# Kernel optimization log

Hardware: AMD Instinct MI355X
Metric: run time of the kernel (lower is better)

The kernel has to match this reference:

```python
import jax, jax.numpy as jnp
import numpy as np

B, DIM, IN_DIM, H, W = 4, 256, 128, 128, 128
DD = IN_DIM // 2          # down_dim = 64
HEADS = 8
BN_EPS = 1e-5


def conv2d(x, w, b=None, pad=0, dil=1):
    y = jax.lax.conv_general_dilated(
        x, w, window_strides=(1, 1),
        padding=[(pad, pad), (pad, pad)],
        rhs_dilation=(dil, dil),
        dimension_numbers=('NCHW', 'OIHW', 'NCHW'))
    if b is not None:
        y = y + b[None, :, None, None]
    return y


def bn_relu(x, s, o):
    # eval-mode BatchNorm2d with running_mean=0, running_var=1
    return jax.nn.relu(x * (s / np.sqrt(1.0 + BN_EPS))[None, :, None, None] + o[None, :, None, None])


def setup_inputs() -> dict:
    ks = iter(jax.random.split(jax.random.key(0), 80))

    def w(shape, sc=0.05):
        return sc * jax.random.normal(next(ks), shape, jnp.float32)

    def s(c):
        return 1.0 + 0.1 * jax.random.normal(next(ks), (c,), jnp.float32)

    def o(c):
        return 0.02 * jax.random.normal(next(ks), (c,), jnp.float32)

    d = {}
    d['x'] = jax.random.normal(next(ks), (B, DIM, H, W), jnp.float32)
    d['w_dc'] = w((IN_DIM, DIM, 3, 3)); d['b_dc'] = w((IN_DIM,)); d['s_dc'] = s(IN_DIM); d['o_dc'] = o(IN_DIM)
    d['w1'] = w((DD, IN_DIM, 1, 1)); d['b1'] = w((DD,)); d['s1'] = s(DD); d['o1'] = o(DD)
    d['w2'] = w((DD, DD, 3, 3)); d['b2'] = w((DD,)); d['s2'] = s(DD); d['o2'] = o(DD)
    d['w3'] = w((DD, DD, 3, 3)); d['b3'] = w((DD,)); d['s3'] = s(DD); d['o3'] = o(DD)
    d['w4'] = w((DD, DD, 3, 3)); d['b4'] = w((DD,)); d['s4'] = s(DD); d['o4'] = o(DD)
    d['w5'] = w((DD, IN_DIM, 1, 1)); d['b5'] = w((DD,)); d['s5'] = s(DD); d['o5'] = o(DD)
    d['temperature'] = jnp.ones((HEADS, 1, 1), jnp.float32)
    d['w_po'] = w((DD, 2 * DD, 1, 1))  # project_out, bias=False
    d['w_wa'] = w((DD // 16, DD, 1, 1)); d['b_wa'] = w((DD // 16,)); d['s_wa'] = s(DD // 16); d['o_wa'] = o(DD // 16)
    d['w_wb'] = w((DD, DD // 16, 1, 1)); d['b_wb'] = w((DD,))
    d['w_f'] = w((DD, 5 * DD, 1, 1)); d['b_f'] = w((DD,)); d['s_f'] = s(DD); d['o_f'] = o(DD)
    d['w_oa'] = w((DD // 2, DD, 3, 3)); d['b_oa'] = w((DD // 2,)); d['s_oa'] = s(DD // 2); d['o_oa'] = o(DD // 2)
    d['w_ob'] = w((1, DD // 2, 1, 1)); d['b_ob'] = w((1,))
    return d


def reference(x, w_dc, b_dc, s_dc, o_dc, w1, b1, s1, o1, w2, b2, s2, o2,
              w3, b3, s3, o3, w4, b4, s4, o4, w5, b5, s5, o5,
              temperature, w_po, w_wa, b_wa, s_wa, o_wa, w_wb, b_wb,
              w_f, b_f, s_f, o_f, w_oa, b_oa, s_oa, o_oa, w_ob, b_ob):

    def branch(c):
        b, ch, h, wd = c.shape
        f = jnp.fft.fft2(c)                                   # [b,ch,h,w] complex64 (q=k=v=tepqkv)
        qkv = f.reshape(b, HEADS, ch // HEADS, h * wd)        # v (unnormalized)
        n = jnp.sqrt(jnp.sum(jnp.square(jnp.abs(qkv)), axis=-1, keepdims=True))
        qn = qkv / jnp.maximum(n, 1e-12)                      # F.normalize(dim=-1); q == k
        attn = jnp.einsum('bhcn,bhdn->bhcd', qn, qn) * temperature
        # custom complex normalization: separate real/imag softmax
        attn = jax.lax.complex(jax.nn.softmax(attn.real, axis=-1),
                               jax.nn.softmax(attn.imag, axis=-1))
        of = jnp.abs(jnp.fft.ifft2(jnp.einsum('bhcd,bhdn->bhcn', attn, qkv)))  # ifft2 over (c, hw)
        of = of.reshape(b, ch, h, wd)
        g = jax.nn.sigmoid(conv2d(bn_relu(conv2d(f.real, w_wa, b_wa), s_wa, o_wa), w_wb, b_wb))
        ol = jnp.abs(jnp.fft.ifft2(g * f))                    # ifft2 over (h, w)
        return conv2d(jnp.concatenate([of, ol], axis=1), w_po) + c

    xd = bn_relu(conv2d(x, w_dc, b_dc, pad=1), s_dc, o_dc)
    c1 = bn_relu(conv2d(xd, w1, b1), s1, o1)
    c2 = bn_relu(conv2d(c1, w2, b2, pad=3, dil=3), s2, o2)
    F2 = branch(c2)
    c3 = bn_relu(conv2d(c1 + F2, w3, b3, pad=5, dil=5), s3, o3)
    F3 = branch(c3)
    c4 = bn_relu(conv2d(c1 + F3, w4, b4, pad=7, dil=7), s4, o4)
    F4 = branch(c4)
    # conv5: global avg pool -> 1x1 conv -> bilinear upsample of a 1x1 map == broadcast
    c5 = bn_relu(conv2d(jnp.mean(xd, axis=(2, 3), keepdims=True), w5, b5), s5, o5)
    c5 = jnp.broadcast_to(c5, (c5.shape[0], c5.shape[1], xd.shape[2], xd.shape[3]))
    fused = bn_relu(conv2d(jnp.concatenate([c1, F2, F3, F4, c5], axis=1), w_f, b_f), s_f, o_f)
    return conv2d(bn_relu(conv2d(fused, w_oa, b_oa, pad=1), s_oa, o_oa), w_ob, b_ob)
```

## Files before the change

kernel.cpp:

```cpp
#include <hip/hip_runtime.h>

#define S 16384
#define PI_F 3.14159265358979f

struct Ptrs { const float* p[43]; };

enum : int {
  O_SBDC=0, O_SB1=256, O_SB2=512, O_SB3=768, O_SB4=1024, O_SB5=1280,
  O_SBWA=1536, O_SBF=1792, O_SBOA=2048,
  O_M=2304, O_C5=2816, O_NRM=3072, O_GRAM=3328, O_ATT2=7424, O_BEFF=11520,
  O_WB=16384,
  O_PART=147456,
  O_H=180224,
  O_WP=442368,
  O_A=524288,
  O_FIN=8912896,
  O_CC=25690112,
  O_DRE=29884416, O_DIMG=34078720,
  O_ERE=38273024, O_EIM=42467328,
  O_G=46661632
};

typedef short bfrag __attribute__((ext_vector_type(8)));
typedef float ffrag __attribute__((ext_vector_type(4)));

__device__ __forceinline__ float bf2f(unsigned short u){
  union { unsigned int i; float f; } v; v.i = ((unsigned int)u) << 16; return v.f;
}
__device__ __forceinline__ unsigned short f2bf(float f){
  unsigned int x = __float_as_uint(f);
  unsigned int r = x + 0x7fffu + ((x >> 16) & 1u);
  return (unsigned short)(r >> 16);
}

__global__ void prep_sb_kernel(Ptrs P, float* ws){
  const float r = rsqrtf(1.0f + 1e-5f);
  int bi=0, si=0, oi=0, C=0, dst=0;
  switch (blockIdx.x){
    case 0: bi=2; si=3; oi=4; C=128; dst=O_SBDC; break;
    case 1: bi=6; si=7; oi=8; C=64; dst=O_SB1; break;
    case 2: bi=10; si=11; oi=12; C=64; dst=O_SB2; break;
    case 3: bi=14; si=15; oi=16; C=64; dst=O_SB3; break;
    case 4: bi=18; si=19; oi=20; C=64; dst=O_SB4; break;
    case 5: bi=22; si=23; oi=24; C=64; dst=O_SB5; break;
    case 6: bi=28; si=29; oi=30; C=4;  dst=O_SBWA; break;
    case 7: bi=34; si=35; oi=36; C=64; dst=O_SBF; break;
    default: bi=38; si=39; oi=40; C=32; dst=O_SBOA; break;
  }
  for (int c = threadIdx.x; c < C; c += 256){
    float bb = P.p[bi][c], ss = P.p[si][c], oo = P.p[oi][c];
    float sc = ss * r;
    ws[dst + c] = sc;
    ws[dst + C + c] = bb * sc + oo;
  }
}

__global__ __launch_bounds__(256) void xpad_kernel(const float* __restrict__ x,
    unsigned short* __restrict__ XT){
  int yy = blockIdx.x, b = blockIdx.y;
  long obase = ((long)(b*130) + yy) * (130L*256);
  int tid = threadIdx.x;
  if (yy == 0 || yy == 129){
    uint4 z; z.x=0; z.y=0; z.z=0; z.w=0;
    for (int i = tid; i < 130*256/8; i += 256)
      *(uint4*)(XT + obase + (long)i*8) = z;
    return;
  }
  __shared__ float LT[64][129];
  int y = yy - 1;
  for (int c0 = 0; c0 < 256; c0 += 64){
    for (int idx = tid; idx < 64*128; idx += 256){
      int ci = idx >> 7, xx = idx & 127;
      LT[ci][xx] = x[((long)(b*256 + c0 + ci)*128 + y)*128 + xx];
    }
    __syncthreads();
    for (int idx = tid; idx < 128*16; idx += 256){
      int xp = idx >> 4, c4 = (idx & 15)*4;
      ushort4 v;
      v.x = f2bf(LT[c4][xp]);   v.y = f2bf(LT[c4+1][xp]);
      v.z = f2bf(LT[c4+2][xp]); v.w = f2bf(LT[c4+3][xp]);
      *(ushort4*)(XT + obase + (long)(xp+1)*256 + c0 + c4) = v;
    }
    __syncthreads();
  }
  if (tid < 64){
    ushort4 z; z.x=0; z.y=0; z.z=0; z.w=0;
    *(ushort4*)(XT + obase + tid*4) = z;
    *(ushort4*)(XT + obase + 129L*256 + tid*4) = z;
  }
}

__global__ void wt_kernel(const float* __restrict__ w, unsigned short* __restrict__ WH,
    unsigned short* __restrict__ WL){
  for (int e = blockIdx.x*256 + threadIdx.x; e < 294912; e += gridDim.x*256){
    int c32 = e & 31, co = (e >> 5) & 127, kc = (e >> 12) & 7, sh = e >> 15;
    int ky = sh / 3, kx = sh - ky*3;
    int ci = kc*32 + c32;
    float v = w[((long)(co*256 + ci)*3 + ky)*3 + kx];
    unsigned short h = f2bf(v);
    WH[e] = h;
    WL[e] = f2bf(v - bf2f(h));
  }
}

__global__ void wtg_kernel(Ptrs P, unsigned short* __restrict__ WB){
  const float* w; int cout; long off;
  switch (blockIdx.y){
    case 0: w = P.p[9];  cout = 64; off = 0;      break;
    case 1: w = P.p[13]; cout = 64; off = 73728;  break;
    case 2: w = P.p[17]; cout = 64; off = 147456; break;
    default: w = P.p[37]; cout = 32; off = 221184; break;
  }
  int total = 576*cout;
  unsigned short* WH = WB + off;
  unsigned short* WL = WH + total;
  for (int e = blockIdx.x*256 + threadIdx.x; e < total; e += gridDim.x*256){
    int c32 = e & 31;
    int co = (e >> 5) & (cout - 1);
    int kc = (e / (32*cout)) & 1;
    int sh = e / (64*cout);
    int ky = sh/3, kx = sh - ky*3;
    int ci = kc*32 + c32;
    float v = w[((long)(co*64 + ci)*3 + ky)*3 + kx];
    unsigned short h = f2bf(v);
    WH[e] = h;
    WL[e] = f2bf(v - bf2f(h));
  }
}

__global__ void wtp_kernel(Ptrs P, unsigned short* __restrict__ WP){
  const float* w; int KC, wstr; long off;
  switch (blockIdx.y){
    case 0: w = P.p[5];  KC = 4; wstr = 128; off = 0;     break;
    case 1: w = P.p[26]; KC = 4; wstr = 128; off = 16384; break;
    default: w = P.p[33]; KC = 8; wstr = 320; off = 32768; break;
  }
  int total = KC*64*32;
  unsigned short* WH = WP + off;
  unsigned short* WL = WH + total;
  for (int e = blockIdx.x*256 + threadIdx.x; e < total; e += gridDim.x*256){
    int c32 = e & 31, co = (e >> 5) & 63, kc = e >> 11;
    float v = w[(long)co*wstr + kc*32 + c32];
    unsigned short h = f2bf(v);
    WH[e] = h;
    WL[e] = f2bf(v - bf2f(h));
  }
}

template<int DIL>
__global__ __launch_bounds__(256) void xpad64_kernel(const float* __restrict__ in1,
    const float* __restrict__ in2, long in_bs, unsigned short* __restrict__ XP){
  constexpr int TW = 128 + 2*DIL;
  int yy = blockIdx.x, b = blockIdx.y;
  long obase = (long)(b*TW + yy) * TW * 64;
  int tid = threadIdx.x;
  if (yy < DIL || yy >= 128 + DIL){
    uint4 z; z.x=0; z.y=0; z.z=0; z.w=0;
    for (int i = tid; i < TW*8; i += 256)
      *(uint4*)(XP + obase + (long)i*8) = z;
    return;
  }
  __shared__ float LT[64][129];
  int y = yy - DIL;
  const float* p1 = in1 + (long)b*in_bs + (long)y*128;
  const float* p2 = in2 ? in2 + (long)b*in_bs + (long)y*128 : nullptr;
  for (int idx = tid; idx < 64*128; idx += 256){
    int ci = idx >> 7, xx = idx & 127;
    float v = p1[(long)ci*S + xx];
    if (p2) v += p2[(long)ci*S + xx];
    LT[ci][xx] = v;
  }
  __syncthreads();
  for (int i = tid; i < 2*DIL*16; i += 256){
    int side = i / (DIL*16);
    int r = i - side*(DIL*16);
    int xcol = side ? (128 + DIL + (r >> 4)) : (r >> 4);
    ushort4 z; z.x=0; z.y=0; z.z=0; z.w=0;
    *(ushort4*)(XP + obase + (long)xcol*64 + (r & 15)*4) = z;
  }
  for (int idx = tid; idx < 128*16; idx += 256){
    int xp = idx >> 4, c4 = (idx & 15)*4;
    ushort4 v;
    v.x = f2bf(LT[c4][xp]);   v.y = f2bf(LT[c4+1][xp]);
    v.z = f2bf(LT[c4+2][xp]); v.w = f2bf(LT[c4+3][xp]);
    *(ushort4*)(XP + obase + (long)(xp + DIL)*64 + c4) = v;
  }
}

template<int DIL, int KC, int NBLK>
__global__ __launch_bounds__(256) void conv3x3_mfma_kernel(
    const unsigned short* __restrict__ XP,
    const unsigned short* __restrict__ WH, const unsigned short* __restrict__ WL,
    const float* __restrict__ scbi, float* __restrict__ out){
  constexpr int CIN = KC*32;
  constexpr int TW = 128 + 2*DIL;
  constexpr int NJ = NBLK/32;
  constexpr int LDA = 36;
  __shared__ unsigned short As[TW*LDA];
  int bid = blockIdx.x;
  int y = (bid & 7)*16 + ((bid >> 3) & 15);
  int b = (bid >> 7) & 3;
  int n2 = bid >> 9;
  int nb = gridDim.x >> 9; if (nb == 0) nb = 1;
  int coutTotal = nb * NBLK;
  int tid = threadIdx.x, wv = tid >> 6, lane = tid & 63;
  int mhalf = wv & 1, nhalf = wv >> 1;
  int px0 = mhalf*64;
  ffrag acc[4][NJ];
  #pragma unroll
  for (int i = 0; i < 4; i++)
    #pragma unroll
    for (int j = 0; j < NJ; j++)
      #pragma unroll
      for (int r = 0; r < 4; r++) acc[i][j][r] = 0.f;

  int kq = (lane >> 4)*8, rown = lane & 15;
  int sx = tid >> 2, sq = tid & 3;
  int cobase = n2*NBLK + nhalf*(NBLK/2);

  for (int ky = 0; ky < 3; ky++){
    long rowbase = ((long)(b*TW + y + ky*DIL))*TW*CIN;
    for (int kc = 0; kc < KC; kc++){
      __syncthreads();
      for (int x = sx; x < TW; x += 64){
        uint4 v = *(const uint4*)(XP + rowbase + (long)x*CIN + kc*32 + sq*8);
        *(uint4*)&As[x*LDA + sq*8] = v;
      }
      __syncthreads();
      #pragma unroll
      for (int kx = 0; kx < 3; kx++){
        int step = (ky*3 + kx)*KC + kc;
        bfrag bhf[NJ], blf[NJ];
        #pragma unroll
        for (int j = 0; j < NJ; j++){
          long wb = ((long)step*coutTotal + cobase + j*16 + rown)*32 + kq;
          bhf[j] = *(const bfrag*)(WH + wb);
          blf[j] = *(const bfrag*)(WL + wb);
        }
        bfrag af[4];
        #pragma unroll
        for (int i = 0; i < 4; i++){
          int x = px0 + i*16 + rown + kx*DIL;
          af[i] = *(const bfrag*)&As[x*LDA + kq];
        }
        #pragma unroll
        for (int i = 0; i < 4; i++)
          #pragma unroll
          for (int j = 0; j < NJ; j++){
            acc[i][j] = __builtin_amdgcn_mfma_f32_16x16x32_bf16(af[i], blf[j], acc[i][j], 0, 0, 0);
            acc[i][j] = __builtin_amdgcn_mfma_f32_16x16x32_bf16(af[i], bhf[j], acc[i][j], 0, 0, 0);
          }
      }
    }
  }
  #pragma unroll
  for (int i = 0; i < 4; i++){
    int pixel = px0 + i*16 + (lane >> 4)*4;
    #pragma unroll
    for (int j = 0; j < NJ; j++){
      int co = cobase + j*16 + (lane & 15);
      float sc = scbi[co], bb = scbi[coutTotal + co];
      float* op = out + ((long)(b*coutTotal + co))*S + y*128 + pixel;
      #pragma unroll
      for (int r = 0; r < 4; r++)
        op[r] = fmaxf(acc[i][j][r]*sc + bb, 0.f);
    }
  }
}

template<int MODE, int KC, int BF16IN>
__global__ __launch_bounds__(256) void conv1x1_mfma_kernel(
    const void* __restrict__ inv, long in_bs,
    const unsigned short* __restrict__ WH, const unsigned short* __restrict__ WL,
    const float* __restrict__ scbi, const float* __restrict__ beff,
    const float* __restrict__ res, long res_bs,
    float* __restrict__ out, long out_bs){
  constexpr int LDA = 36;
  __shared__ unsigned short Als[128*LDA];
  __shared__ unsigned short BHs[64*LDA];
  __shared__ unsigned short BLs[64*LDA];
  int bid = blockIdx.x;
  int y = (bid & 7)*16 + ((bid >> 3) & 15);
  int b = bid >> 7;
  int tid = threadIdx.x, wv = tid >> 6, lane = tid & 63;
  int mt0 = (wv & 1)*4, nt0 = (wv >> 1)*2;
  ffrag acc[4][2];
  #pragma unroll
  for (int i = 0; i < 4; i++)
    #pragma unroll
    for (int j = 0; j < 2; j++)
      #pragma unroll
      for (int r = 0; r < 4; r++) acc[i][j][r] = 0.f;
  int pq = tid & 31, cg = tid >> 5;
  int kq = (lane >> 4)*8, rown = lane & 15;
  int wrB = (tid >> 2)*LDA + (tid & 3)*8;
  const float* ibf = (const float*)inv + (long)b*in_bs + y*128;
  const unsigned short* ibs = (const unsigned short*)inv + (long)b*in_bs + y*128;
  unsigned short a[16];
  uint4 BHr, BLr;
  #pragma unroll
  for (int cc = 0; cc < 4; cc++)
    #pragma unroll
    for (int i = 0; i < 4; i++){
      if (BF16IN) a[cc*4 + i] = ibs[(long)(cg*4 + cc)*S + pq + 32*i];
      else        a[cc*4 + i] = f2bf(ibf[(long)(cg*4 + cc)*S + pq + 32*i]);
    }
  BHr = *(const uint4*)(WH + tid*8);
  BLr = *(const uint4*)(WL + tid*8);
  for (int kc = 0; kc < KC; kc++){
    __syncthreads();
    #pragma unroll
    for (int i = 0; i < 4; i++){
      ushort4 v;
      v.x = a[0 + i];  v.y = a[4 + i];
      v.z = a[8 + i];  v.w = a[12 + i];
      *(ushort4*)&Als[(pq + 32*i)*LDA + cg*4] = v;
    }
    *(uint4*)&BHs[wrB] = BHr;
    *(uint4*)&BLs[wrB] = BLr;
    __syncthreads();
    if (kc + 1 < KC){
      #pragma unroll
      for (int cc = 0; cc < 4; cc++)
        #pragma unroll
        for (int i = 0; i < 4; i++){
          long off = (long)((kc + 1)*32 + cg*4 + cc)*S + pq + 32*i;
          if (BF16IN) a[cc*4 + i] = ibs[off];
          else        a[cc*4 + i] = f2bf(ibf[off]);
        }
      long gw = (long)(kc + 1)*2048;
      BHr = *(const uint4*)(WH + gw + tid*8);
      BLr = *(const uint4*)(WL + gw + tid*8);
    }
    bfrag af[4], bhf[2], blf[2];
    #pragma unroll
    for (int i = 0; i < 4; i++)
      af[i] = *(const bfrag*)&Als[((mt0 + i)*16 + rown)*LDA + kq];
    #pragma unroll
    for (int j = 0; j < 2; j++){
      bhf[j] = *(const bfrag*)&BHs[((nt0 + j)*16 + rown)*LDA + kq];
      blf[j] = *(const bfrag*)&BLs[((nt0 + j)*16 + rown)*LDA + kq];
    }
    #pragma unroll
    for (int i = 0; i < 4; i++)
      #pragma unroll
      for (int j = 0; j < 2; j++){
        acc[i][j] = __builtin_amdgcn_mfma_f32_16x16x32_bf16(af[i], blf[j], acc[i][j], 0, 0, 0);
        acc[i][j] = __builtin_amdgcn_mfma_f32_16x16x32_bf16(af[i], bhf[j], acc[i][j], 0, 0, 0);
      }
  }
  #pragma unroll
  for (int i = 0; i < 4; i++){
    int pixel = (mt0 + i)*16 + (lane >> 4)*4;
    #pragma unroll
    for (int j = 0; j < 2; j++){
      int co = (nt0 + j)*16 + (lane & 15);
      float* op = out + (long)b*out_bs + (long)co*S + y*128 + pixel;
      #pragma unroll
      for (int r = 0; r < 4; r++){
        float v = acc[i][j][r];
        if (MODE == 0){
          v = fmaxf(v*scbi[co] + scbi[64 + co], 0.f);
        } else if (MODE == 1){
          v += res[(long)b*res_bs + (long)co*S + y*128 + pixel + r];
        } else {
          v = fmaxf(v*scbi[co] + beff[b*64 + co], 0.f);
        }
        op[r] = v;
      }
    }
  }
}

__device__ __forceinline__ void fft128_mk_tw(float (&tws)[8], float (&twc)[8],
                                             float sign, int lane){
  float a0 = sign * (2.0f*PI_F/128.0f) * (float)lane;
  __sincosf(a0, &tws[0], &twc[0]);
  int i = 1;
  #pragma unroll
  for (int h = 32; h >= 1; h >>= 1, i++){
    int j = lane & (h - 1);
    float a = sign * (2.0f*PI_F/128.0f) * (float)(j * (64/h));
    __sincosf(a, &tws[i], &twc[i]);
  }
}

__device__ __forceinline__ void fft128(float& z0r, float& z0i, float& z1r, float& z1i,
    const float (&tws)[8], const float (&twc)[8], int lane){
  {
    float ar = z0r, ai = z0i, br = z1r, bi = z1i;
    z0r = ar + br; z0i = ai + bi;
    float dr = ar - br, di = ai - bi;
    float s = tws[0], c = twc[0];
    z1r = dr*c - di*s; z1i = dr*s + di*c;
  }
  int idx = 1;
  #pragma unroll
  for (int h = 32; h >= 1; h >>= 1, idx++){
    float s = tws[idx], c = twc[idx];
    bool up = (lane & h) != 0;
    float pr, pi, nr, ni;
    pr = __shfl_xor(z0r, h, 64); pi = __shfl_xor(z0i, h, 64);
    if (!up){ nr = z0r + pr; ni = z0i + pi; }
    else { float dr = pr - z0r, di = pi - z0i; nr = dr*c - di*s; ni = dr*s + di*c; }
    z0r = nr; z0i = ni;
    pr = __shfl_xor(z1r, h, 64); pi = __shfl_xor(z1i, h, 64);
    if (!up){ nr = z1r + pr; ni = z1i + pi; }
    else { float dr = pr - z1r, di = pi - z1i; nr = dr*c - di*s; ni = dr*s + di*c; }
    z1r = nr; z1i = ni;
  }
}


__global__ __launch_bounds__(1024) void fft2_fwd_kernel(const float* __restrict__ in,
    unsigned short* __restrict__ outRe, unsigned short* __restrict__ outIm){
  __shared__ float lre[128][129];
  __shared__ float lim[128][129];
  int plane = blockIdx.x;
  int tid = threadIdx.x, wv = tid >> 6, lane = tid & 63;
  long pbase = (long)plane * S;
  for (int i = tid; i < S/4; i += 1024){
    int px = i*4; int r = px >> 7, c = px & 127;
    float4 v = *(const float4*)(in + pbase + px);
    lre[r][c] = v.x; lre[r][c+1] = v.y; lre[r][c+2] = v.z; lre[r][c+3] = v.w;
  }
  float tws[8], twc[8];
  fft128_mk_tw(tws, twc, -1.0f, lane);
  __syncthreads();
  #pragma unroll
  for (int rr = 0; rr < 8; rr++){
    int r = wv*8 + rr;
    float z0r = lre[r][lane], z0i = 0.f;
    float z1r = lre[r][lane + 64], z1i = 0.f;
    fft128(z0r, z0i, z1r, z1i, tws, twc, lane);
    int k = __brev(lane) >> 25;
    lre[r][k] = z0r;     lim[r][k] = z0i;
    lre[r][k+1] = z1r;   lim[r][k+1] = z1i;
  }
  __syncthreads();
  #pragma unroll
  for (int cc = 0; cc < 8; cc++){
    int c = wv*8 + cc;
    float z0r = lre[lane][c], z0i = lim[lane][c];
    float z1r = lre[lane + 64][c], z1i = lim[lane + 64][c];
    fft128(z0r, z0i, z1r, z1i, tws, twc, lane);
    int k = __brev(lane) >> 25;
    lre[k][c] = z0r;     lim[k][c] = z0i;
    lre[k+1][c] = z1r;   lim[k+1][c] = z1i;
  }
  __syncthreads();
  for (int i = tid; i < S/2; i += 1024){
    int px = i*2; int r = px >> 7, c = px & 127;
    ushort2 vr, vi;
    vr.x = f2bf(lre[r][c]); vr.y = f2bf(lre[r][c+1]);
    vi.x = f2bf(lim[r][c]); vi.y = f2bf(lim[r][c+1]);
    *(ushort2*)(outRe + pbase + px) = vr;
    *(ushort2*)(outIm + pbase + px) = vi;
  }
}

__global__ __launch_bounds__(1024) void ifft2_gate_abs_ol_kernel(
    const unsigned short* __restrict__ Dre, const unsigned short* __restrict__ Dim,
    const float* __restrict__ H, const float* __restrict__ wb, const float* __restrict__ bwb,
    unsigned short* __restrict__ AB){
  __shared__ float lre[128][129];
  __shared__ float lim[128][129];
  int plane = blockIdx.x;
  int b = plane >> 6, ch = plane & 63;
  int tid = threadIdx.x, wv = tid >> 6, lane = tid & 63;
  long pbase = (long)plane * S;
  float w0 = wb[ch*4], w1 = wb[ch*4+1], w2 = wb[ch*4+2], w3 = wb[ch*4+3];
  float bw = bwb[ch];
  const float* Hb = H + (long)b*4*S;
  for (int i = tid; i < S; i += 1024){
    int r = i >> 7, c = i & 127;
    float hv = bw + w0*Hb[i] + w1*Hb[S + i] + w2*Hb[2*S + i] + w3*Hb[3*S + i];
    float g = 1.0f / (1.0f + __expf(-hv));
    lre[r][c] = bf2f(Dre[pbase + i]) * g;
    lim[r][c] = bf2f(Dim[pbase + i]) * g;
  }
  float tws[8], twc[8];
  fft128_mk_tw(tws, twc, 1.0f, lane);
  __syncthreads();
  #pragma unroll
  for (int cc = 0; cc < 8; cc++){
    int c = wv*8 + cc;
    float z0r = lre[lane][c], z0i = lim[lane][c];
    float z1r = lre[lane + 64][c], z1i = lim[lane + 64][c];
    fft128(z0r, z0i, z1r, z1i, tws, twc, lane);
    int k = __brev(lane) >> 25;
    lre[k][c] = z0r;     lim[k][c] = z0i;
    lre[k+1][c] = z1r;   lim[k+1][c] = z1i;
  }
  __syncthreads();
  unsigned short* out = AB + ((long)(b*128 + 64 + ch)) * S;
  #pragma unroll
  for (int rr = 0; rr < 8; rr++){
    int r = wv*8 + rr;
    float z0r = lre[r][lane], z0i = lim[r][lane];
    float z1r = lre[r][lane + 64], z1i = lim[r][lane + 64];
    fft128(z0r, z0i, z1r, z1i, tws, twc, lane);
    int k = __brev(lane) >> 25;
    ushort2 v;
    v.x = f2bf(sqrtf(z0r*z0r + z0i*z0i) * (1.0f/16384.0f));
    v.y = f2bf(sqrtf(z1r*z1r + z1i*z1i) * (1.0f/16384.0f));
    *(ushort2*)(out + (long)r*128 + k) = v;
  }
}

__global__ __launch_bounds__(1024) void ifft2_attn_abs_ofT_kernel(
    const unsigned short* __restrict__ Dre, const unsigned short* __restrict__ Dim,
    const float* __restrict__ ATT2, unsigned short* __restrict__ AB){
  __shared__ float lre[128][129];
  __shared__ float lim[128][129];
  int plane = blockIdx.x;
  int b = plane >> 6, ch = plane & 63;
  int bh = plane >> 3;
  int cp = plane & 7;
  int tid = threadIdx.x, wv = tid >> 6, lane = tid & 63;
  long hbase = (long)bh * 8 * S;
  float wr[8], wi[8];
  #pragma unroll
  for (int d = 0; d < 8; d++){
    wr[d] = ATT2[bh*128 + (cp*8 + d)*2];
    wi[d] = ATT2[bh*128 + (cp*8 + d)*2 + 1];
  }
  for (int i = tid; i < S/2; i += 1024){
    int px = i*2;
    float sr0=0.f, si0=0.f, sr1=0.f, si1=0.f;
    #pragma unroll
    for (int d = 0; d < 8; d++){
      ushort2 ur = *(const ushort2*)(Dre + hbase + (long)d*S + px);
      ushort2 ui = *(const ushort2*)(Dim + hbase + (long)d*S + px);
      float xr0 = bf2f(ur.x), xi0 = bf2f(ui.x);
      float xr1 = bf2f(ur.y), xi1 = bf2f(ui.y);
      sr0 += wr[d]*xr0 - wi[d]*xi0;  si0 += wr[d]*xi0 + wi[d]*xr0;
      sr1 += wr[d]*xr1 - wi[d]*xi1;  si1 += wr[d]*xi1 + wi[d]*xr1;
    }
    int r = px >> 7, c = px & 127;
    lre[r][c] = sr0;   lim[r][c] = si0;
    lre[r][c+1] = sr1; lim[r][c+1] = si1;
  }
  float tws[8], twc[8];
  fft128_mk_tw(tws, twc, 1.0f, lane);
  __syncthreads();
  #pragma unroll
  for (int cc = 0; cc < 8; cc++){
    int c = wv*8 + cc;
    float z0r = lre[lane][c], z0i = lim[lane][c];
    float z1r = lre[lane + 64][c], z1i = lim[lane + 64][c];
    fft128(z0r, z0i, z1r, z1i, tws, twc, lane);
    int k = __brev(lane) >> 25;
    float s, co;
    float a0 = (2.0f*PI_F/16384.0f) * (float)(c * k);
    __sincosf(a0, &s, &co);
    float t = z0r*co - z0i*s; z0i = z0r*s + z0i*co; z0r = t;
    float a1 = (2.0f*PI_F/16384.0f) * (float)(c * (k + 1));
    __sincosf(a1, &s, &co);
    t = z1r*co - z1i*s; z1i = z1r*s + z1i*co; z1r = t;
    lre[k][c] = z0r;     lim[k][c] = z0i;
    lre[k+1][c] = z1r;   lim[k+1][c] = z1i;
  }
  __syncthreads();
  float absv[8][2];
  #pragma unroll
  for (int rr = 0; rr < 8; rr++){
    int r = wv*8 + rr;
    float z0r = lre[r][lane], z0i = lim[r][lane];
    float z1r = lre[r][lane + 64], z1i = lim[r][lane + 64];
    fft128(z0r, z0i, z1r, z1i, tws, twc, lane);
    absv[rr][0] = sqrtf(z0r*z0r + z0i*z0i) * (1.0f/16384.0f);
    absv[rr][1] = sqrtf(z1r*z1r + z1i*z1i) * (1.0f/16384.0f);
  }
  __syncthreads();
  int k2 = __brev(lane) >> 25;
  #pragma unroll
  for (int rr = 0; rr < 8; rr++){
    int r = wv*8 + rr;
    lre[k2][r] = absv[rr][0];
    lre[k2+1][r] = absv[rr][1];
  }
  __syncthreads();
  unsigned short* out = AB + ((long)(b*128 + ch)) * S;
  for (int i = tid; i < S/2; i += 1024){
    int px = i*2; int r = px >> 7, c = px & 127;
    ushort2 v;
    v.x = f2bf(lre[r][c]); v.y = f2bf(lre[r][c+1]);
    *(ushort2*)(out + px) = v;
  }
}

__global__ __launch_bounds__(256) void gram_part_kernel(
    const unsigned short* __restrict__ Dre, const unsigned short* __restrict__ Dim,
    float* __restrict__ PART){
  int bh = blockIdx.x, slab = blockIdx.y;
  long base = (long)bh * 8 * S;
  int n0 = slab * 2048;
  float accr[36], acci[36], nsq[8];
  #pragma unroll
  for (int i = 0; i < 36; i++){ accr[i] = 0.f; acci[i] = 0.f; }
  #pragma unroll
  for (int i = 0; i < 8; i++) nsq[i] = 0.f;
  for (int it = 0; it < 8; it++){
    int n = n0 + it*256 + threadIdx.x;
    float xr[8], xi[8];
    #pragma unroll
    for (int c = 0; c < 8; c++){
      xr[c] = bf2f(Dre[base + (long)c*S + n]);
      xi[c] = bf2f(Dim[base + (long)c*S + n]);
      nsq[c] += xr[c]*xr[c] + xi[c]*xi[c];
    }
    int t = 0;
    #pragma unroll
    for (int c = 0; c < 8; c++)
      #pragma unroll
      for (int d = c; d < 8; d++){
        accr[t] += xr[c]*xr[d] - xi[c]*xi[d];
        acci[t] += xr[c]*xi[d] + xi[c]*xr[d];
        t++;
      }
  }
  __shared__ float red[4][80];
  int wv = threadIdx.x >> 6, lane = threadIdx.x & 63;
  #pragma unroll
  for (int i = 0; i < 80; i++){
    float v = (i < 36) ? accr[i] : (i < 72) ? acci[i - 36] : nsq[i - 72];
    #pragma unroll
    for (int o = 32; o; o >>= 1) v += __shfl_xor(v, o, 64);
    if (lane == 0) red[wv][i] = v;
  }
  __syncthreads();
  if (threadIdx.x < 80){
    int i = threadIdx.x;
    PART[(long)(bh*8 + slab)*80 + i] = red[0][i] + red[1][i] + red[2][i] + red[3][i];
  }
}

__global__ void attn2f_kernel(const float* __restrict__ PART,
    const float* __restrict__ temp, float* __restrict__ ATT2){
  __shared__ float ssum[80];
  __shared__ float sar[64], sai[64];
  int bh = blockIdx.x;
  int t = threadIdx.x;
  if (t < 80){
    float s = 0.f;
    for (int i = 0; i < 8; i++) s += PART[(long)(bh*8 + i)*80 + t];
    ssum[t] = s;
  }
  __syncthreads();
  if (t >= 64) return;
  int lane = t;
  int c = lane >> 3, d = lane & 7;
  int lo = min(c, d), hi = max(c, d);
  int t2 = lo*8 - lo*(lo - 1)/2 + (hi - lo);
  float nnc = fmaxf(sqrtf(ssum[72 + c]), 1e-12f);
  float nnd = fmaxf(sqrtf(ssum[72 + d]), 1e-12f);
  float inv = temp[bh & 7] / (nnc * nnd);
  float ar = ssum[t2] * inv, ai = ssum[36 + t2] * inv;
  float m = ar;
  m = fmaxf(m, __shfl_xor(m, 1, 64)); m = fmaxf(m, __shfl_xor(m, 2, 64)); m = fmaxf(m, __shfl_xor(m, 4, 64));
  float e = __expf(ar - m);
  float su = e;
  su += __shfl_xor(su, 1, 64); su += __shfl_xor(su, 2, 64); su += __shfl_xor(su, 4, 64);
  ar = e / su;
  m = ai;
  m = fmaxf(m, __shfl_xor(m, 1, 64)); m = fmaxf(m, __shfl_xor(m, 2, 64)); m = fmaxf(m, __shfl_xor(m, 4, 64));
  e = __expf(ai - m);
  su = e;
  su += __shfl_xor(su, 1, 64); su += __shfl_xor(su, 2, 64); su += __shfl_xor(su, 4, 64);
  ai = e / su;
  sar[lane] = ar; sai[lane] = ai;
  __syncthreads();
  const float ct[8] = {1.f, 0.70710678f, 0.f, -0.70710678f, -1.f, -0.70710678f, 0.f, 0.70710678f};
  const float st[8] = {0.f, 0.70710678f, 1.f, 0.70710678f, 0.f, -0.70710678f, -1.f, -0.70710678f};
  int cp = c;
  float sr = 0.f, si = 0.f;
  #pragma unroll
  for (int cc = 0; cc < 8; cc++){
    int k = (cc * cp) & 7;
    float a = sar[cc*8 + d], b2 = sai[cc*8 + d];
    sr += ct[k]*a - st[k]*b2;
    si += ct[k]*b2 + st[k]*a;
  }
  float2 v; v.x = sr * 0.125f; v.y = si * 0.125f;
  ((float2*)ATT2)[bh*64 + lane] = v;
}

__global__ __launch_bounds__(256) void gateh_kernel(const unsigned short* __restrict__ Dre,
    const float* __restrict__ wa, const float* __restrict__ sbwa, float* __restrict__ H){
  int b = blockIdx.y;
  int px = blockIdx.x*256 + threadIdx.x;
  long base = (long)b * 64 * S + px;
  float h0 = 0.f, h1 = 0.f, h2 = 0.f, h3 = 0.f;
  for (int ci = 0; ci < 64; ci++){
    float x = bf2f(Dre[base + (long)ci*S]);
    h0 += wa[ci]*x; h1 += wa[64 + ci]*x; h2 += wa[128 + ci]*x; h3 += wa[192 + ci]*x;
  }
  long ob = (long)b * 4 * S + px;
  H[ob]       = fmaxf(h0*sbwa[0] + sbwa[4], 0.f);
  H[ob + S]   = fmaxf(h1*sbwa[1] + sbwa[5], 0.f);
  H[ob + 2*S] = fmaxf(h2*sbwa[2] + sbwa[6], 0.f);
  H[ob + 3*S] = fmaxf(h3*sbwa[3] + sbwa[7], 0.f);
}

__global__ __launch_bounds__(256) void mean_kernel(const float* __restrict__ A, float* __restrict__ M){
  int p = blockIdx.x;
  long base = (long)p * S;
  float s = 0.f;
  for (int n = threadIdx.x; n < S; n += 256) s += A[base + n];
  #pragma unroll
  for (int o = 32; o; o >>= 1) s += __shfl_xor(s, o, 64);
  __shared__ float sm[4];
  if ((threadIdx.x & 63) == 0) sm[threadIdx.x >> 6] = s;
  __syncthreads();
  if (threadIdx.x == 0) M[p] = (sm[0] + sm[1] + sm[2] + sm[3]) * (1.0f/16384.0f);
}

__global__ void c5_kernel(const float* __restrict__ W5, const float* __restrict__ sb5,
    const float* __restrict__ M, float* __restrict__ C5){
  int t = threadIdx.x;
  if (t >= 256) return;
  int b = t >> 6, co = t & 63;
  float s = 0.f;
  for (int ci = 0; ci < 128; ci++) s += W5[co*128 + ci] * M[b*128 + ci];
  C5[t] = fmaxf(s * sb5[co] + sb5[64 + co], 0.f);
}

__global__ void beff_kernel(const float* __restrict__ WF, const float* __restrict__ sbf,
    const float* __restrict__ C5, float* __restrict__ BEFF){
  int t = threadIdx.x;
  if (t >= 256) return;
  int b = t >> 6, co = t & 63;
  float s = 0.f;
  for (int j = 0; j < 64; j++) s += WF[co*320 + 256 + j] * C5[b*64 + j];
  BEFF[t] = s * sbf[co] + sbf[64 + co];
}

__global__ __launch_bounds__(256) void ob_kernel(const float* __restrict__ Tin,
    const float* __restrict__ wob, const float* __restrict__ bob, float* __restrict__ out){
  int b = blockIdx.y;
  int px = blockIdx.x*1024 + (threadIdx.x & 63)*4 + (threadIdx.x >> 6)*256;
  float b0 = bob[0];
  float4 a; a.x = b0; a.y = b0; a.z = b0; a.w = b0;
  for (int ci = 0; ci < 32; ci++){
    float4 v = *(const float4*)(Tin + ((long)b*32 + ci)*S + px);
    float w = wob[ci];
    a.x += w*v.x; a.y += w*v.y; a.z += w*v.z; a.w += w*v.w;
  }
  *(float4*)(out + (long)b*S + px) = a;
}

extern "C" void kernel_launch(void* const* d_in, const int* in_sizes, int n_in,
                              void* d_out, int out_size, void* d_ws, size_t ws_size,
                              hipStream_t stream){
  float* ws = (float*)d_ws;
  Ptrs P;
  for (int i = 0; i < 43 && i < n_in; i++) P.p[i] = (const float*)d_in[i];
  float* out = (float*)d_out;

  float* A   = ws + O_A;
  float* FIN = ws + O_FIN;
  float* CC  = ws + O_CC;
  float* G   = ws + O_G;
  float* H   = ws + O_H;

  unsigned short* DRE16 = (unsigned short*)(ws + O_DRE);
  unsigned short* DIM16 = (unsigned short*)(ws + O_DIMG);
  unsigned short* AB    = (unsigned short*)(ws + O_A);

  unsigned short* XT  = (unsigned short*)(ws + O_DRE);
  unsigned short* WHd = (unsigned short*)(ws + O_CC);
  unsigned short* WLd = (unsigned short*)(ws + O_CC + 147456);
  unsigned short* WB  = (unsigned short*)(ws + O_WB);
  unsigned short* WP  = (unsigned short*)(ws + O_WP);
  unsigned short* XP  = (unsigned short*)(ws + O_ERE);

  prep_sb_kernel<<<dim3(9), dim3(256), 0, stream>>>(P, ws);
  xpad_kernel<<<dim3(130, 4), dim3(256), 0, stream>>>(P.p[0], XT);
  wt_kernel<<<dim3(128), dim3(256), 0, stream>>>(P.p[1], WHd, WLd);
  wtg_kernel<<<dim3(16, 4), dim3(256), 0, stream>>>(P, WB);
  wtp_kernel<<<dim3(8, 3), dim3(256), 0, stream>>>(P, WP);

  conv3x3_mfma_kernel<1,8,64><<<dim3(1024), dim3(256), 0, stream>>>(
      XT, WHd, WLd, ws + O_SBDC, A);

  mean_kernel<<<dim3(512), dim3(256), 0, stream>>>(A, ws + O_M);
  c5_kernel<<<dim3(1), dim3(256), 0, stream>>>(P.p[21], ws + O_SB5, ws + O_M, ws + O_C5);
  beff_kernel<<<dim3(1), dim3(256), 0, stream>>>(P.p[33], ws + O_SBF, ws + O_C5, ws + O_BEFF);

  conv1x1_mfma_kernel<0,4,0><<<dim3(512), dim3(256), 0, stream>>>(
      A, 128*S, WP, WP + 8192, ws + O_SB1, nullptr, nullptr, 0, FIN, 256*S);

  for (int k = 0; k < 3; k++){
    const float* sb = ws + (k == 0 ? O_SB2 : k == 1 ? O_SB3 : O_SB4);
    const float* in2 = (k == 0) ? nullptr : FIN + (long)(64*k)*S;
    unsigned short* wh = WB + (k == 0 ? 0 : k == 1 ? 73728 : 147456);
    if (k == 0){
      xpad64_kernel<3><<<dim3(134, 4), dim3(256), 0, stream>>>(FIN, in2, 256*S, XP);
      conv3x3_mfma_kernel<3,2,32><<<dim3(1024), dim3(256), 0, stream>>>(
          XP, wh, wh + 36864, sb, CC);
    } else if (k == 1){
      xpad64_kernel<5><<<dim3(138, 4), dim3(256), 0, stream>>>(FIN, in2, 256*S, XP);
      conv3x3_mfma_kernel<5,2,32><<<dim3(1024), dim3(256), 0, stream>>>(
          XP, wh, wh + 36864, sb, CC);
    } else {
      xpad64_kernel<7><<<dim3(142, 4), dim3(256), 0, stream>>>(FIN, in2, 256*S, XP);
      conv3x3_mfma_kernel<7,2,32><<<dim3(1024), dim3(256), 0, stream>>>(
          XP, wh, wh + 36864, sb, CC);
    }

    fft2_fwd_kernel<<<dim3(256), dim3(1024), 0, stream>>>(CC, DRE16, DIM16);
    gram_part_kernel<<<dim3(32, 8), dim3(256), 0, stream>>>(DRE16, DIM16, ws + O_PART);
    attn2f_kernel<<<dim3(32), dim3(128), 0, stream>>>(ws + O_PART, P.p[25], ws + O_ATT2);
    gateh_kernel<<<dim3(64, 4), dim3(256), 0, stream>>>(DRE16, P.p[27], ws + O_SBWA, H);
    ifft2_gate_abs_ol_kernel<<<dim3(256), dim3(1024), 0, stream>>>(
        DRE16, DIM16, H, P.p[31], P.p[32], AB);
    ifft2_attn_abs_ofT_kernel<<<dim3(256), dim3(1024), 0, stream>>>(
        DRE16, DIM16, ws + O_ATT2, AB);
    conv1x1_mfma_kernel<1,4,1><<<dim3(512), dim3(256), 0, stream>>>(
        AB, 128*S, WP + 16384, WP + 24576, nullptr, nullptr, CC, 64*S,
        FIN + (long)(64*(k + 1))*S, 256*S);
  }

  conv1x1_mfma_kernel<2,8,0><<<dim3(512), dim3(256), 0, stream>>>(
      FIN, 256*S, WP + 32768, WP + 49152, ws + O_SBF, ws + O_BEFF, nullptr, 0, CC, 64*S);
  xpad64_kernel<1><<<dim3(130, 4), dim3(256), 0, stream>>>(CC, nullptr, 64*S, XP);
  conv3x3_mfma_kernel<1,2,32><<<dim3(512), dim3(256), 0, stream>>>(
      XP, WB + 221184, WB + 221184 + 18432, ws + O_SBOA, G);
  ob_kernel<<<dim3(16, 4), dim3(256), 0, stream>>>(G, P.p[41], P.p[42], out);
}
```

Baseline: 921.7 us.

## Register-prefetch next conv3x3 input tile and widen dilated convs to 64 outputs

The conv3x3 MFMA kernel now loads the next (ky,kc) input row slice from global memory into registers while the MFMAs for the current slice run, then writes it to LDS at the next step. This hides global load latency behind compute. The dilated 64-channel convs also switch to NBLK=64 with half the grid, so each block computes all 64 output channels and reads each input row once instead of twice. The cost is higher register pressure (prefetch buffers plus more accumulators) and fewer blocks to fill the GPU.

Result: slower. 974.9 us (+5.8%).

```diff
diff --git a/kernel.cpp b/kernel.cpp
--- a/kernel.cpp
+++ b/kernel.cpp
@@ -196,6 +196,7 @@
   constexpr int TW = 128 + 2*DIL;
   constexpr int NJ = NBLK/32;
   constexpr int LDA = 36;
+  constexpr int NSTG = (TW + 63)/64;
   __shared__ unsigned short As[TW*LDA];
   int bid = blockIdx.x;
   int y = (bid & 7)*16 + ((bid >> 3) & 15);
@@ -218,39 +219,56 @@
   int sx = tid >> 2, sq = tid & 3;
   int cobase = n2*NBLK + nhalf*(NBLK/2);
 
-  for (int ky = 0; ky < 3; ky++){
-    long rowbase = ((long)(b*TW + y + ky*DIL))*TW*CIN;
-    for (int kc = 0; kc < KC; kc++){
-      __syncthreads();
-      for (int x = sx; x < TW; x += 64){
-        uint4 v = *(const uint4*)(XP + rowbase + (long)x*CIN + kc*32 + sq*8);
-        *(uint4*)&As[x*LDA + sq*8] = v;
+  uint4 pre[NSTG];
+  {
+    long rowbase = ((long)(b*TW + y))*TW*CIN + sq*8;
+    #pragma unroll
+    for (int t = 0; t < NSTG; t++){
+      int x = sx + 64*t;
+      if (x < TW) pre[t] = *(const uint4*)(XP + rowbase + (long)x*CIN);
+    }
+  }
+  for (int s = 0; s < 3*KC; s++){
+    int ky = s / KC, kc = s - ky*KC;
+    __syncthreads();
+    #pragma unroll
+    for (int t = 0; t < NSTG; t++){
+      int x = sx + 64*t;
+      if (x < TW) *(uint4*)&As[x*LDA + sq*8] = pre[t];
+    }
+    __syncthreads();
+    if (s + 1 < 3*KC){
+      int s2 = s + 1, ky2 = s2 / KC, kc2 = s2 - ky2*KC;
+      long rowbase = ((long)(b*TW + y + ky2*DIL))*TW*CIN + kc2*32 + sq*8;
+      #pragma unroll
+      for (int t = 0; t < NSTG; t++){
+        int x = sx + 64*t;
+        if (x < TW) pre[t] = *(const uint4*)(XP + rowbase + (long)x*CIN);
       }
-      __syncthreads();
-      #pragma unroll
-      for (int kx = 0; kx < 3; kx++){
-        int step = (ky*3 + kx)*KC + kc;
-        bfrag bhf[NJ], blf[NJ];
+    }
+    #pragma unroll
+    for (int kx = 0; kx < 3; kx++){
+      int step = (ky*3 + kx)*KC + kc;
+      bfrag bhf[NJ], blf[NJ];
+      #pragma unroll
+      for (int j = 0; j < NJ; j++){
+        long wb = ((long)step*coutTotal + cobase + j*16 + rown)*32 + kq;
+        bhf[j] = *(const bfrag*)(WH + wb);
+        blf[j] = *(const bfrag*)(WL + wb);
+      }
+      bfrag af[4];
+      #pragma unroll
+      for (int i = 0; i < 4; i++){
+        int x = px0 + i*16 + rown + kx*DIL;
+        af[i] = *(const bfrag*)&As[x*LDA + kq];
+      }
+      #pragma unroll
+      for (int i = 0; i < 4; i++)
         #pragma unroll
         for (int j = 0; j < NJ; j++){
-          long wb = ((long)step*coutTotal + cobase + j*16 + rown)*32 + kq;
-          bhf[j] = *(const bfrag*)(WH + wb);
-          blf[j] = *(const bfrag*)(WL + wb);
+          acc[i][j] = __builtin_amdgcn_mfma_f32_16x16x32_bf16(af[i], blf[j], acc[i][j], 0, 0, 0);
+          acc[i][j] = __builtin_amdgcn_mfma_f32_16x16x32_bf16(af[i], bhf[j], acc[i][j], 0, 0, 0);
         }
-        bfrag af[4];
-        #pragma unroll
-        for (int i = 0; i < 4; i++){
-          int x = px0 + i*16 + rown + kx*DIL;
-          af[i] = *(const bfrag*)&As[x*LDA + kq];
-        }
-        #pragma unroll
-        for (int i = 0; i < 4; i++)
-          #pragma unroll
-          for (int j = 0; j < NJ; j++){
-            acc[i][j] = __builtin_amdgcn_mfma_f32_16x16x32_bf16(af[i], blf[j], acc[i][j], 0, 0, 0);
-            acc[i][j] = __builtin_amdgcn_mfma_f32_16x16x32_bf16(af[i], bhf[j], acc[i][j], 0, 0, 0);
-          }
-      }
     }
   }
   #pragma unroll
@@ -797,15 +815,15 @@
     unsigned short* wh = WB + (k == 0 ? 0 : k == 1 ? 73728 : 147456);
     if (k == 0){
       xpad64_kernel<3><<<dim3(134, 4), dim3(256), 0, stream>>>(FIN, in2, 256*S, XP);
-      conv3x3_mfma_kernel<3,2,32><<<dim3(1024), dim3(256), 0, stream>>>(
+      conv3x3_mfma_kernel<3,2,64><<<dim3(512), dim3(256), 0, stream>>>(
           XP, wh, wh + 36864, sb, CC);
     } else if (k == 1){
       xpad64_kernel<5><<<dim3(138, 4), dim3(256), 0, stream>>>(FIN, in2, 256*S, XP);
-      conv3x3_mfma_kernel<5,2,32><<<dim3(1024), dim3(256), 0, stream>>>(
+      conv3x3_mfma_kernel<5,2,64><<<dim3(512), dim3(256), 0, stream>>>(
           XP, wh, wh + 36864, sb, CC);
     } else {
       xpad64_kernel<7><<<dim3(142, 4), dim3(256), 0, stream>>>(FIN, in2, 256*S, XP);
-      conv3x3_mfma_kernel<7,2,32><<<dim3(1024), dim3(256), 0, stream>>>(
+      conv3x3_mfma_kernel<7,2,64><<<dim3(512), dim3(256), 0, stream>>>(
           XP, wh, wh + 36864, sb, CC);
     }
 
```
